# Performance work log

Measured on AMD Instinct MI355X. Metric: run time of the kernel, lower is better.

## Reference

```python
import jax, jax.numpy as jnp
import numpy as np

N_NODES = 100_000
N_EDGES = 6_400_000
D_FEAT = 128
NUM_BASIS = 10
MAX_RADIUS = 2.0
EPS = 1e-12
# e3nn soft_one_hot_linspace 'smooth_finite' constant: 1.14136 * e^2
_SMOOTH_C = float(1.14136 * np.exp(2.0))
_SQRT3 = float(np.sqrt(3.0))


def _sus(x):
    # e3nn sus(x) = exp(-1/x) for x > 0 else 0 (smooth compactly-supported bump factor)
    xs = jnp.where(x > 0.0, x, 1.0)  # safe denominator
    return jnp.where(x > 0.0, jnp.exp(-1.0 / xs), 0.0)


def _soft_one_hot_smooth_finite(x, end, number):
    # e3nn soft_one_hot_linspace(start=0, end, number, basis='smooth_finite', cutoff=True)
    step = end / (number + 1)
    values = step * jnp.arange(1, number + 1, dtype=x.dtype)  # linspace(0,end,number+2)[1:-1]
    diff = (x[..., None] - values) / step  # [E, number]
    return _SMOOTH_C * _sus(diff + 1.0) * _sus(1.0 - diff)


def _spherical_harmonics_lmax2(v):
    # e3nn o3.spherical_harmonics, lmax=2, normalization='norm' (each l-block has unit
    # norm for unit input). v: [E,3] unit vectors, e3nn (x, y, z) convention.
    x, y, z = v[..., 0], v[..., 1], v[..., 2]
    return jnp.stack([
        jnp.ones_like(x),              # l=0
        x, y, z,                       # l=1
        _SQRT3 * x * z,                # l=2, m components (e3nn order)
        _SQRT3 * x * y,
        y * y - 0.5 * (x * x + z * z),
        _SQRT3 * y * z,
        0.5 * _SQRT3 * (z * z - x * x),
    ], axis=-1)  # [E, 9]


def setup_inputs() -> dict:
    key = jax.random.key(0)
    k1, k2, k3 = jax.random.split(key, 3)
    feature = jax.random.normal(k1, (N_NODES, D_FEAT), dtype=jnp.float32)
    pos = jax.random.normal(k2, (N_NODES, 3), dtype=jnp.float32)
    edge = jax.random.randint(k3, (2, N_EDGES), 0, N_NODES, dtype=jnp.int64)
    max_neighbor_radius = jnp.float32(MAX_RADIUS)
    return {"feature": feature, "pos": pos,
            "max_neighbor_radius": max_neighbor_radius, "edge": edge}


def reference(feature, pos, max_neighbor_radius, edge):
    edge_src, edge_dst = edge[0], edge[1]
    edge_vec = pos[edge_dst] - pos[edge_src]               # [E, 3] gather + sub
    edge_length = jnp.linalg.norm(edge_vec, axis=-1)       # [E]
    # smooth_finite radial embedding, scaled by sqrt(number_of_basis)
    edge_length_embedded = _soft_one_hot_smooth_finite(
        edge_length, max_neighbor_radius, NUM_BASIS) * float(np.sqrt(NUM_BASIS))
    # normalize=True: unit vectors (F.normalize semantics: x / max(|x|, eps))
    unit = edge_vec / jnp.maximum(edge_length, EPS)[..., None]
    edge_sh = _spherical_harmonics_lmax2(unit)             # [E, 9]
    return edge_length_embedded, edge_sh
```

## Files before the change

kernel.cpp:

```cpp
#include <hip/hip_runtime.h>
#include <hip/hip_bf16.h>


#define TILE 256

__global__ __launch_bounds__(256) void pack_pos_kernel(
    const float* __restrict__ pos, float4* __restrict__ pos4, int N)
{
    int i = blockIdx.x * 256 + threadIdx.x;
    if (i < N) {
        pos4[i] = make_float4(pos[3 * i + 0], pos[3 * i + 1], pos[3 * i + 2], 0.0f);
    }
}

__global__ __launch_bounds__(TILE) void edge_sh_kernel(
    const int*    __restrict__ edge,
    const float4* __restrict__ pos4,
    const float*  __restrict__ radius,
    float*        __restrict__ out,
    int E)
{
    __shared__ __align__(16) float lds[TILE * 10 + TILE * 9];
    float* lds_emb = lds;
    float* lds_sh  = lds + TILE * 10;

    const int tid = threadIdx.x;
    const long long base_e = (long long)blockIdx.x * TILE;
    const long long e = base_e + tid;
    const bool valid = (e < (long long)E);

    const float end = radius[0];
    const float inv_step = 11.0f / end;

    float vx = 0.0f, vy = 0.0f, vz = 0.0f;
    if (valid) {
        int s = edge[e];
        int d = edge[(long long)E + e];
        float4 a = pos4[s];
        float4 b = pos4[d];
        vx = b.x - a.x; vy = b.y - a.y; vz = b.z - a.z;
    }

    float len2 = vx * vx + vy * vy + vz * vz;
    float len  = sqrtf(len2);

    const float ls = len * inv_step;
    #pragma unroll
    for (int j = 0; j < 10; ++j) {
        float d = ls - (float)(j + 1);
        float t = __builtin_fmaf(-d, d, 1.0f);
        float val = (t > 0.0f)
                  ? 26.669299714f * __expf(__fdividef(-2.0f, t))
                  : 0.0f;
        if (!valid) val = 0.0f;
        lds_emb[tid * 10 + j] = val;
    }

    float inv = 1.0f / fmaxf(len, 1e-12f);
    float x = vx * inv, y = vy * inv, z = vz * inv;
    const float S3 = 1.7320508075688772f;
    lds_sh[tid * 9 + 0] = valid ? 1.0f : 0.0f;
    lds_sh[tid * 9 + 1] = x;
    lds_sh[tid * 9 + 2] = y;
    lds_sh[tid * 9 + 3] = z;
    lds_sh[tid * 9 + 4] = S3 * x * z;
    lds_sh[tid * 9 + 5] = S3 * x * y;
    lds_sh[tid * 9 + 6] = y * y - 0.5f * (x * x + z * z);
    lds_sh[tid * 9 + 7] = S3 * y * z;
    lds_sh[tid * 9 + 8] = 0.5f * S3 * (z * z - x * x);

    __syncthreads();

    const long long rem_edges = (long long)E - base_e;
    const int n_emb4 = (int)((rem_edges >= TILE ? (long long)TILE * 10
                                                : rem_edges * 10) / 4);
    const int n_sh4  = (int)((rem_edges >= TILE ? (long long)TILE * 9
                                                : rem_edges * 9 ) / 4);

    float4* g_emb = (float4*)(out + base_e * 10);
    const float4* l_emb = (const float4*)lds_emb;
    #pragma unroll
    for (int i = 0; i < 3; ++i) {
        int idx = tid + i * TILE;
        if (idx < n_emb4) g_emb[idx] = l_emb[idx];
    }

    float4* g_sh = (float4*)(out + (long long)E * 10 + base_e * 9);
    const float4* l_sh = (const float4*)lds_sh;
    #pragma unroll
    for (int i = 0; i < 3; ++i) {
        int idx = tid + i * TILE;
        if (idx < n_sh4) g_sh[idx] = l_sh[idx];
    }
}

extern "C" void kernel_launch(void* const* d_in, const int* in_sizes, int n_in,
                              void* d_out, int out_size, void* d_ws, size_t ws_size,
                              hipStream_t stream) {
    const float* pos    = (const float*)d_in[1];
    const float* radius = (const float*)d_in[2];
    const int*   edge   = (const int*)d_in[3];
    float*       out    = (float*)d_out;

    const int N = in_sizes[1] / 3;
    const int E = in_sizes[3] / 2;

    float4* pos4 = (float4*)d_ws;

    hipLaunchKernelGGL(pack_pos_kernel, dim3((N + 255) / 256), dim3(256), 0, stream,
                       pos, pos4, N);

    const int nblk = (E + TILE - 1) / TILE;
    hipLaunchKernelGGL(edge_sh_kernel, dim3(nblk), dim3(TILE), 0, stream,
                       edge, pos4, radius, out, E);
}
```

Measured before the change: 610.3 us.

## Process four edges per thread with direct vector stores, dropping LDS staging

Each thread now handles four consecutive edges. It loads their indices with int4 loads, issues eight independent position gathers, and writes the 40 embedding floats and 36 SH floats straight to global memory as 16-byte vector stores. This removes the shared-memory staging buffer and the __syncthreads, and gives each thread more memory-level parallelism. In exchange, each thread's stores are spread across contiguous 160- and 144-byte chunks, so lanes in a wave write to strided addresses rather than fully coalesced lines. Register pressure also rises and fewer threads are launched.

```diff
diff --git a/kernel.cpp b/kernel.cpp
--- a/kernel.cpp
+++ b/kernel.cpp
@@ -3,6 +3,9 @@
 
 
 #define TILE 256
+#define EPT 4
+
+typedef float nfloat4 __attribute__((ext_vector_type(4)));
 
 __global__ __launch_bounds__(256) void pack_pos_kernel(
     const float* __restrict__ pos, float4* __restrict__ pos4, int N)
@@ -13,6 +16,31 @@
     }
 }
 
+__device__ __forceinline__ void edge_math(float vx, float vy, float vz,
+                                          float inv_step, float* em10, float* sh9)
+{
+    float len = sqrtf(vx * vx + vy * vy + vz * vz);
+    float ls  = len * inv_step;
+    #pragma unroll
+    for (int j = 0; j < 10; ++j) {
+        float d = ls - (float)(j + 1);
+        float t = __builtin_fmaf(-d, d, 1.0f);
+        em10[j] = (t > 0.0f)
+                ? 26.669299714f * __expf(__fdividef(-2.0f, t))
+                : 0.0f;
+    }
+    float inv = 1.0f / fmaxf(len, 1e-12f);
+    float x = vx * inv, y = vy * inv, z = vz * inv;
+    const float S3 = 1.7320508075688772f;
+    sh9[0] = 1.0f;
+    sh9[1] = x;  sh9[2] = y;  sh9[3] = z;
+    sh9[4] = S3 * x * z;
+    sh9[5] = S3 * x * y;
+    sh9[6] = y * y - 0.5f * (x * x + z * z);
+    sh9[7] = S3 * y * z;
+    sh9[8] = 0.5f * S3 * (z * z - x * x);
+}
+
 __global__ __launch_bounds__(TILE) void edge_sh_kernel(
     const int*    __restrict__ edge,
     const float4* __restrict__ pos4,
@@ -20,77 +48,59 @@
     float*        __restrict__ out,
     int E)
 {
-    __shared__ __align__(16) float lds[TILE * 10 + TILE * 9];
-    float* lds_emb = lds;
-    float* lds_sh  = lds + TILE * 10;
+    const long long t  = (long long)blockIdx.x * TILE + threadIdx.x;
+    const long long e0 = t * EPT;
+    if (e0 >= (long long)E) return;
 
-    const int tid = threadIdx.x;
-    const long long base_e = (long long)blockIdx.x * TILE;
-    const long long e = base_e + tid;
-    const bool valid = (e < (long long)E);
+    const float inv_step = 11.0f / radius[0];
 
-    const float end = radius[0];
-    const float inv_step = 11.0f / end;
+    if (e0 + EPT <= (long long)E) {
+        int4 s4 = *(const int4*)(edge + e0);
+        int4 d4 = *(const int4*)(edge + (long long)E + e0);
+        const int si[4] = {s4.x, s4.y, s4.z, s4.w};
+        const int di[4] = {d4.x, d4.y, d4.z, d4.w};
 
-    float vx = 0.0f, vy = 0.0f, vz = 0.0f;
-    if (valid) {
-        int s = edge[e];
-        int d = edge[(long long)E + e];
-        float4 a = pos4[s];
-        float4 b = pos4[d];
-        vx = b.x - a.x; vy = b.y - a.y; vz = b.z - a.z;
-    }
+        float vx[4], vy[4], vz[4];
+        #pragma unroll
+        for (int k = 0; k < 4; ++k) {
+            float4 a = pos4[si[k]];
+            float4 b = pos4[di[k]];
+            vx[k] = b.x - a.x; vy[k] = b.y - a.y; vz[k] = b.z - a.z;
+        }
 
-    float len2 = vx * vx + vy * vy + vz * vz;
-    float len  = sqrtf(len2);
+        float em[40], sh[36];
+        #pragma unroll
+        for (int k = 0; k < 4; ++k) {
+            edge_math(vx[k], vy[k], vz[k], inv_step, &em[k * 10], &sh[k * 9]);
+        }
 
-    const float ls = len * inv_step;
-    #pragma unroll
-    for (int j = 0; j < 10; ++j) {
-        float d = ls - (float)(j + 1);
-        float t = __builtin_fmaf(-d, d, 1.0f);
-        float val = (t > 0.0f)
-                  ? 26.669299714f * __expf(__fdividef(-2.0f, t))
-                  : 0.0f;
-        if (!valid) val = 0.0f;
-        lds_emb[tid * 10 + j] = val;
-    }
-
-    float inv = 1.0f / fmaxf(len, 1e-12f);
-    float x = vx * inv, y = vy * inv, z = vz * inv;
-    const float S3 = 1.7320508075688772f;
-    lds_sh[tid * 9 + 0] = valid ? 1.0f : 0.0f;
-    lds_sh[tid * 9 + 1] = x;
-    lds_sh[tid * 9 + 2] = y;
-    lds_sh[tid * 9 + 3] = z;
-    lds_sh[tid * 9 + 4] = S3 * x * z;
-    lds_sh[tid * 9 + 5] = S3 * x * y;
-    lds_sh[tid * 9 + 6] = y * y - 0.5f * (x * x + z * z);
-    lds_sh[tid * 9 + 7] = S3 * y * z;
-    lds_sh[tid * 9 + 8] = 0.5f * S3 * (z * z - x * x);
-
-    __syncthreads();
-
-    const long long rem_edges = (long long)E - base_e;
-    const int n_emb4 = (int)((rem_edges >= TILE ? (long long)TILE * 10
-                                                : rem_edges * 10) / 4);
-    const int n_sh4  = (int)((rem_edges >= TILE ? (long long)TILE * 9
-                                                : rem_edges * 9 ) / 4);
-
-    float4* g_emb = (float4*)(out + base_e * 10);
-    const float4* l_emb = (const float4*)lds_emb;
-    #pragma unroll
-    for (int i = 0; i < 3; ++i) {
-        int idx = tid + i * TILE;
-        if (idx < n_emb4) g_emb[idx] = l_emb[idx];
-    }
-
-    float4* g_sh = (float4*)(out + (long long)E * 10 + base_e * 9);
-    const float4* l_sh = (const float4*)lds_sh;
-    #pragma unroll
-    for (int i = 0; i < 3; ++i) {
-        int idx = tid + i * TILE;
-        if (idx < n_sh4) g_sh[idx] = l_sh[idx];
+        nfloat4* ge = (nfloat4*)(out + e0 * 10);
+        #pragma unroll
+        for (int i = 0; i < 10; ++i) {
+            nfloat4 v = {em[4 * i], em[4 * i + 1], em[4 * i + 2], em[4 * i + 3]};
+            ge[i] = v;
+        }
+        nfloat4* gs = (nfloat4*)(out + (long long)E * 10 + e0 * 9);
+        #pragma unroll
+        for (int i = 0; i < 9; ++i) {
+            nfloat4 v = {sh[4 * i], sh[4 * i + 1], sh[4 * i + 2], sh[4 * i + 3]};
+            gs[i] = v;
+        }
+    } else {
+        for (long long e = e0; e < (long long)E; ++e) {
+            int s = edge[e];
+            int d = edge[(long long)E + e];
+            float4 a = pos4[s];
+            float4 b = pos4[d];
+            float em10[10], sh9[9];
+            edge_math(b.x - a.x, b.y - a.y, b.z - a.z, inv_step, em10, sh9);
+            float* pe = out + e * 10;
+            #pragma unroll
+            for (int j = 0; j < 10; ++j) pe[j] = em10[j];
+            float* ps = out + (long long)E * 10 + e * 9;
+            #pragma unroll
+            for (int k = 0; k < 9; ++k) ps[k] = sh9[k];
+        }
     }
 }
 
@@ -110,7 +120,8 @@
     hipLaunchKernelGGL(pack_pos_kernel, dim3((N + 255) / 256), dim3(256), 0, stream,
                        pos, pos4, N);
 
-    const int nblk = (E + TILE - 1) / TILE;
+    const long long threads = ((long long)E + EPT - 1) / EPT;
+    const int nblk = (int)((threads + TILE - 1) / TILE);
     hipLaunchKernelGGL(edge_sh_kernel, dim3(nblk), dim3(TILE), 0, stream,
                        edge, pos4, radius, out, E);
 }
```

After: 657.5 us. 7.7% more time.
